# Performance work log

Hardware: AMD Instinct MI355X
Metric: run time of the kernel (lower is better)

Reference implementation:

```python
import jax, jax.numpy as jnp
import numpy as np

V, N, C, H, W = 4, 65536, 128, 512, 512
M_POOL, K, DH = 1024, 5, 128


def setup_inputs() -> dict:
    key = jax.random.key(0)
    ks = jax.random.split(key, 6)
    points = jax.random.normal(ks[0], (N, 3), dtype=jnp.float32) * 0.3  # human-scale pcd near origin
    zbuffer = 2.0 + jax.random.uniform(ks[1], (V, 1, H, W), dtype=jnp.float32)  # depth ~ camera distance
    feat_map = jax.random.normal(ks[2], (V, C, H, W), dtype=jnp.float32) * 0.1
    image = jax.random.uniform(ks[3], (V, 3, H, W), dtype=jnp.float32)
    # cameras: identity rotation, small x-baseline, looking at origin from z=2.5
    R = jnp.tile(jnp.eye(3, dtype=jnp.float32)[None], (V, 1, 1))
    t = jnp.stack([jnp.array([0.1 * v - 0.15, 0.0, 2.5], dtype=jnp.float32) for v in range(V)])
    extr = jnp.concatenate([R, t[:, :, None]], axis=-1)  # [V,3,4]
    intr = jnp.tile(jnp.array([[700.0, 0.0, W / 2], [0.0, 700.0, H / 2], [0.0, 0.0, 1.0]], dtype=jnp.float32)[None], (V, 1, 1))
    W1 = jax.random.normal(ks[4], (C + 1, DH), dtype=jnp.float32) * 0.05
    b1 = jnp.zeros((DH,), dtype=jnp.float32)
    w2 = jax.random.normal(ks[5], (DH, 1), dtype=jnp.float32) * 0.05
    return dict(points=points, extr=extr, intr=intr, zbuffer=zbuffer,
                feat_map=feat_map, image=image, W1=W1, b1=b1, w2=w2)


def _bilinear(img, u, v):
    """Zero-padded bilinear sample. img [C,H,W]; u,v [N] pixel coords -> [N,C]."""
    Cc, Hh, Ww = img.shape
    u0f = jnp.floor(u); v0f = jnp.floor(v)
    du = u - u0f; dv = v - v0f
    u0 = u0f.astype(jnp.int32); v0 = v0f.astype(jnp.int32)
    out = jnp.zeros((Cc, u.shape[0]), dtype=img.dtype)
    for vi, ui, w in ((v0, u0, (1 - du) * (1 - dv)), (v0, u0 + 1, du * (1 - dv)),
                      (v0 + 1, u0, (1 - du) * dv), (v0 + 1, u0 + 1, du * dv)):
        valid = ((vi >= 0) & (vi < Hh) & (ui >= 0) & (ui < Ww)).astype(img.dtype)
        vals = img[:, jnp.clip(vi, 0, Hh - 1), jnp.clip(ui, 0, Ww - 1)]  # [C,N]
        out = out + vals * (w * valid)[None]
    return out.T  # [N,C]


def _project(points, extr, intr):
    cam = jnp.einsum('vij,nj->vni', extr[:, :, :3], points) + extr[:, None, :, 3]  # [V,N,3]
    depth = cam[..., 2]  # [V,N]
    pix = jnp.einsum('vij,vnj->vni', intr, cam)
    u = pix[..., 0] / (pix[..., 2] + 1e-9)
    v = pix[..., 1] / (pix[..., 2] + 1e-9)
    return u, v, depth


def reference(points, extr, intr, zbuffer, feat_map, image, W1, b1, w2):
    u, v, depth = _project(points, extr, intr)
    sample = jax.vmap(_bilinear)  # over V views
    zbuf = sample(zbuffer, u, v)[..., 0]  # [V,N] sampled z-buffer (0 outside frame)
    out_mask = jnp.any(zbuf == 0.0, axis=0)  # [N] point missing in some view
    # --- KNN inverse-distance zbuf replacement (torch.no_grad block) ---
    pts_sg = jax.lax.stop_gradient(points)
    zbuf_sg = jax.lax.stop_gradient(zbuf)
    cand = pts_sg[:M_POOL]                       # candidate in-point pool
    cand_bad = out_mask[:M_POOL]
    d2 = jnp.sum((pts_sg[:, None, :] - cand[None, :, :]) ** 2, axis=-1)  # [N,M]
    d2 = jnp.where(cand_bad[None, :], jnp.inf, d2)
    negd, idx = jax.lax.top_k(-d2, K)            # K nearest candidates
    dists = jnp.sqrt(jnp.maximum(-negd, 0.0))
    disp = 1.0 / (dists + 1e-8)
    wknn = disp / (jnp.sum(disp, -1, keepdims=True) + 1e-12)  # [N,K]
    replace = jnp.sum(zbuf_sg[:, idx] * wknn[None], -1)       # [V,N]
    zbuf = jnp.where(out_mask[None], replace, zbuf)
    # --- visibility ---
    vis = 1.0 - jnp.abs(zbuf - depth) / (zbuf + 1e-9)  # [V,N]
    # --- multi-view projector sampling + attention fusion (MVF) ---
    feat_s = sample(feat_map, u, v)  # [V,N,C]
    rgb_s = sample(image, u, v)      # [V,N,3]
    x = jnp.concatenate([feat_s, vis[..., None]], -1)          # [V,N,C+1]
    h = jax.nn.relu(jnp.einsum('vnc,cd->vnd', x, W1) + b1)     # [V,N,DH]
    attn = jax.nn.softmax(jnp.einsum('vnd,do->vno', h, w2), axis=0)  # softmax over views
    feat = jnp.sum(attn * feat_s, axis=0)  # [N,C]
    rgb = jnp.sum(attn * rgb_s, axis=0)    # [N,3]
    return jnp.concatenate([feat, rgb], axis=-1)  # [N,C+3]
```

## Files before the change

### kernel.cpp

```cpp
#include <hip/hip_runtime.h>
#include <math.h>

#define NV 4
#define NPT 65536
#define NC 128
#define IMH 512
#define IMW 512
#define MPOOL 1024
#define NDH 128
#define KNN 5
#define NB 4
#define OUTC 131

typedef unsigned int uint32;
typedef unsigned short ushort16;
typedef __attribute__((ext_vector_type(8))) short short8v;
typedef __attribute__((ext_vector_type(4))) float float4v;

__device__ inline ushort16 f2bf(float f) {
    uint32 u = __float_as_uint(f);
    u += 0x7fffu + ((u >> 16) & 1u);
    return (ushort16)(u >> 16);
}
__device__ inline float bflo(uint32 a) { return __uint_as_float(a << 16); }
__device__ inline float bfhi(uint32 a) { return __uint_as_float(a & 0xffff0000u); }
__device__ inline float bf1(ushort16 a) { return __uint_as_float(((uint32)a) << 16); }

__global__ void k_wprep(const float* __restrict__ W1, uint4* __restrict__ Bf,
                        int* __restrict__ counter) {
    int idx = blockIdx.x * blockDim.x + threadIdx.x;
    if (idx == 0) *counter = 0;
    if (idx >= 5 * 8 * 64) return;
    int l = idx & 63, t = (idx >> 6) & 7, kb = idx >> 9;
    int d = t * 16 + (l & 15);
    uint32 w[4];
#pragma unroll
    for (int p = 0; p < 4; ++p) {
        uint32 lohi = 0;
#pragma unroll
        for (int h = 0; h < 2; ++h) {
            int j = p * 2 + h;
            int k = kb * 32 + (l >> 4) * 8 + j;
            float wv = (k < NC + 1) ? W1[k * NDH + d] : 0.f;
            lohi |= ((uint32)f2bf(wv)) << (16 * h);
        }
        w[p] = lohi;
    }
    Bf[idx] = make_uint4(w[0], w[1], w[2], w[3]);
}

__global__ __launch_bounds__(256)
void k_prep(const float* __restrict__ pts, const float* __restrict__ extr,
            const float* __restrict__ intr, const float* __restrict__ zbuffer,
            float* __restrict__ uarr, float* __restrict__ varr,
            float* __restrict__ darr, float* __restrict__ zarr,
            int* __restrict__ mask, int* __restrict__ list,
            int* __restrict__ counter) {
    int n = blockIdx.x * blockDim.x + threadIdx.x;
    if (n >= NPT) return;
    float p0 = pts[3 * n], p1 = pts[3 * n + 1], p2 = pts[3 * n + 2];
    int msk = 0;
#pragma unroll
    for (int v = 0; v < NV; ++v) {
        const float* e = extr + v * 12;
        float c0 = e[0] * p0 + e[1] * p1 + e[2] * p2 + e[3];
        float c1 = e[4] * p0 + e[5] * p1 + e[6] * p2 + e[7];
        float c2 = e[8] * p0 + e[9] * p1 + e[10] * p2 + e[11];
        const float* kk = intr + v * 9;
        float x0 = kk[0] * c0 + kk[1] * c1 + kk[2] * c2;
        float x1 = kk[3] * c0 + kk[4] * c1 + kk[5] * c2;
        float x2 = kk[6] * c0 + kk[7] * c1 + kk[8] * c2;
        float uu = x0 / (x2 + 1e-9f);
        float vv = x1 / (x2 + 1e-9f);
        int vn = v * NPT + n;
        uarr[vn] = uu; varr[vn] = vv; darr[vn] = c2;

        const float* img = zbuffer + (size_t)v * IMH * IMW;
        float u0f = floorf(uu), v0f = floorf(vv);
        float du = uu - u0f, dv = vv - v0f;
        int iu0 = (int)u0f, iv0 = (int)v0f;
        float w00 = (1.f - du) * (1.f - dv);
        float w01 = du * (1.f - dv);
        float w10 = (1.f - du) * dv;
        float w11 = du * dv;
        int iu0c = min(max(iu0, 0), IMW - 1), iu1c = min(max(iu0 + 1, 0), IMW - 1);
        int iv0c = min(max(iv0, 0), IMH - 1), iv1c = min(max(iv0 + 1, 0), IMH - 1);
        float m00 = (iu0 >= 0 && iu0 < IMW && iv0 >= 0 && iv0 < IMH) ? w00 : 0.f;
        float m01 = (iu0 + 1 >= 0 && iu0 + 1 < IMW && iv0 >= 0 && iv0 < IMH) ? w01 : 0.f;
        float m10 = (iu0 >= 0 && iu0 < IMW && iv0 + 1 >= 0 && iv0 + 1 < IMH) ? w10 : 0.f;
        float m11 = (iu0 + 1 >= 0 && iu0 + 1 < IMW && iv0 + 1 >= 0 && iv0 + 1 < IMH) ? w11 : 0.f;
        float z = img[iv0c * IMW + iu0c] * m00 + img[iv0c * IMW + iu1c] * m01 +
                  img[iv1c * IMW + iu0c] * m10 + img[iv1c * IMW + iu1c] * m11;
        zarr[vn] = z;
        msk |= (z == 0.f);
    }
    mask[n] = msk;
    if (msk) {
        int pos = atomicAdd(counter, 1);
        list[pos] = n;
    }
}

__global__ __launch_bounds__(256)
void k_knn_c(const float* __restrict__ pts, const int* __restrict__ mask,
             const int* __restrict__ list, const int* __restrict__ counter,
             float* __restrict__ zarr) {
    __shared__ float cx[MPOOL], cy[MPOOL], cz[MPOOL];
    int count = *counter;
    if ((int)blockIdx.x * 256 >= count) return;
    for (int m = threadIdx.x; m < MPOOL; m += 256) {
        int bad = mask[m];
        cx[m] = bad ? INFINITY : pts[3 * m];
        cy[m] = pts[3 * m + 1];
        cz[m] = pts[3 * m + 2];
    }
    __syncthreads();
    int i = blockIdx.x * 256 + threadIdx.x;
    if (i >= count) return;
    int n = list[i];
    float px = pts[3 * n], py = pts[3 * n + 1], pz = pts[3 * n + 2];
    float bd[KNN];
    int bi[KNN];
#pragma unroll
    for (int k = 0; k < KNN; ++k) { bd[k] = INFINITY; bi[k] = 0; }
    for (int m = 0; m < MPOOL; ++m) {
        float dx = px - cx[m];
        float dy = py - cy[m];
        float dz = pz - cz[m];
        float d = dx * dx + dy * dy + dz * dz;
        int id = m;
#pragma unroll
        for (int k = 0; k < KNN; ++k) {
            if (d < bd[k]) {
                float td = bd[k]; int ti = bi[k];
                bd[k] = d; bi[k] = id;
                d = td; id = ti;
            }
        }
    }
    float disp[KNN];
    float s = 0.f;
#pragma unroll
    for (int k = 0; k < KNN; ++k) {
        float dist = sqrtf(fmaxf(bd[k], 0.f));
        disp[k] = 1.f / (dist + 1e-8f);
        s += disp[k];
    }
    float inv = 1.f / (s + 1e-12f);
#pragma unroll
    for (int v = 0; v < NV; ++v) {
        float r = 0.f;
#pragma unroll
        for (int k = 0; k < KNN; ++k) r += zarr[v * NPT + bi[k]] * (disp[k] * inv);
        zarr[v * NPT + n] = r;
    }
}

__global__ __launch_bounds__(256)
void k_tfeat(const float* __restrict__ feat, ushort16* __restrict__ tfeat) {
    __shared__ ushort16 tile[128][130];
    int bid = blockIdx.x;
    int xt = bid & 3;
    int y = (bid >> 2) & 511;
    int v = bid >> 11;
    int x0 = xt * 128;
    int lane = threadIdx.x & 63, wave = threadIdx.x >> 6;
    const size_t HW = (size_t)IMH * IMW;
    const float* src = feat + (size_t)v * NC * HW + (size_t)y * IMW + x0;
#pragma unroll
    for (int i = 0; i < 32; ++i) {
        int c = i * 4 + wave;
        float2 val = *(const float2*)(src + (size_t)c * HW + lane * 2);
        tile[lane * 2][c] = f2bf(val.x);
        tile[lane * 2 + 1][c] = f2bf(val.y);
    }
    __syncthreads();
    uint32* dst = (uint32*)tfeat + ((size_t)v * HW + (size_t)y * IMW + x0) * 64;
#pragma unroll
    for (int i = 0; i < 32; ++i) {
        int pix = i * 4 + wave;
        uint32 val = *(const uint32*)&tile[pix][2 * lane];
        dst[(size_t)pix * 64 + lane] = val;
    }
}

__global__ __launch_bounds__(256)
void k_trgb(const float* __restrict__ image, ushort16* __restrict__ trgb) {
    int bid = blockIdx.x;
    int xt = bid & 1, y = (bid >> 1) & 511, v = bid >> 10;
    int x = xt * 256 + threadIdx.x;
    const size_t HW = (size_t)IMH * IMW;
    size_t p = (size_t)y * IMW + x;
    const float* src = image + (size_t)v * 3 * HW;
    ushort4 o;
    o.x = f2bf(src[p]);
    o.y = f2bf(src[HW + p]);
    o.z = f2bf(src[2 * HW + p]);
    o.w = 0;
    *(ushort4*)(trgb + ((size_t)v * HW + p) * 4) = o;
}

__global__ __launch_bounds__(128)
void k_fused_m(const float* __restrict__ uarr, const float* __restrict__ varr,
               const float* __restrict__ darr, const float* __restrict__ zarr,
               const ushort16* __restrict__ tfeat, const ushort16* __restrict__ trgb,
               const uint4* __restrict__ Bf, const float* __restrict__ b1,
               const float* __restrict__ w2, float* __restrict__ out) {
    const int tid = threadIdx.x;
    const int n0 = blockIdx.x * NB;
    const size_t HW = (size_t)IMH * IMW;
    __shared__ ushort16 fs[16][168];
    __shared__ float rgbs[16][3];
    __shared__ int po[16][4];
    __shared__ float pm[16][4];
    __shared__ float viss[16];
    __shared__ float sc[16];
    __shared__ float red[16][2];

    if (tid < 16) {
        int nb = tid >> 2, v = tid & 3;
        int vn = v * NPT + n0 + nb;
        float uu = uarr[vn], vv = varr[vn];
        float u0f = floorf(uu), v0f = floorf(vv);
        float du = uu - u0f, dv = vv - v0f;
        int iu0 = (int)u0f, iv0 = (int)v0f;
        float w00 = (1.f - du) * (1.f - dv);
        float w01 = du * (1.f - dv);
        float w10 = (1.f - du) * dv;
        float w11 = du * dv;
        int iu0c = min(max(iu0, 0), IMW - 1), iu1c = min(max(iu0 + 1, 0), IMW - 1);
        int iv0c = min(max(iv0, 0), IMH - 1), iv1c = min(max(iv0 + 1, 0), IMH - 1);
        float m00 = (iu0 >= 0 && iu0 < IMW && iv0 >= 0 && iv0 < IMH) ? w00 : 0.f;
        float m01 = (iu0 + 1 < IMW && iu0 + 1 >= 0 && iv0 >= 0 && iv0 < IMH) ? w01 : 0.f;
        float m10 = (iu0 >= 0 && iu0 < IMW && iv0 + 1 < IMH && iv0 + 1 >= 0) ? w10 : 0.f;
        float m11 = (iu0 + 1 < IMW && iu0 + 1 >= 0 && iv0 + 1 < IMH && iv0 + 1 >= 0) ? w11 : 0.f;
        int o00 = iv0c * IMW + iu0c, o01 = iv0c * IMW + iu1c;
        int o10 = iv1c * IMW + iu0c, o11 = iv1c * IMW + iu1c;
        po[tid][0] = o00; po[tid][1] = o01; po[tid][2] = o10; po[tid][3] = o11;
        pm[tid][0] = m00; pm[tid][1] = m01; pm[tid][2] = m10; pm[tid][3] = m11;
        float z = zarr[vn], dd = darr[vn];
        float vis = 1.f - fabsf(z - dd) / (z + 1e-9f);
        viss[tid] = vis;
        fs[tid][128] = f2bf(vis);
        for (int k = 129; k < 168; ++k) fs[tid][k] = 0;
        const ushort16* rb = trgb + (size_t)v * HW * 4;
        float ar = 0.f, ag = 0.f, ab = 0.f;
        int oo[4] = {o00, o01, o10, o11};
        float mm[4] = {m00, m01, m10, m11};
#pragma unroll
        for (int k = 0; k < 4; ++k) {
            const ushort16* c = rb + (size_t)oo[k] * 4;
            ar += bf1(c[0]) * mm[k];
            ag += bf1(c[1]) * mm[k];
            ab += bf1(c[2]) * mm[k];
        }
        rgbs[tid][0] = ar; rgbs[tid][1] = ag; rgbs[tid][2] = ab;
    }
    __syncthreads();

    const uint32* T = (const uint32*)tfeat;
    int sub = tid >> 6, c2 = tid & 63;
#pragma unroll
    for (int i = 0; i < 8; ++i) {
        int q = i * 2 + sub;
        int v = q & 3;
        const uint32* Bv = T + (size_t)v * HW * 64;
        int o0 = po[q][0], o1 = po[q][1], o2 = po[q][2], o3 = po[q][3];
        float m0 = pm[q][0], m1 = pm[q][1], m2 = pm[q][2], m3 = pm[q][3];
        uint32 a0 = Bv[(size_t)o0 * 64 + c2];
        uint32 a1 = Bv[(size_t)o1 * 64 + c2];
        uint32 a2 = Bv[(size_t)o2 * 64 + c2];
        uint32 a3 = Bv[(size_t)o3 * 64 + c2];
        float lo = bflo(a0) * m0 + bflo(a1) * m1 + bflo(a2) * m2 + bflo(a3) * m3;
        float hi = bfhi(a0) * m0 + bfhi(a1) * m1 + bfhi(a2) * m2 + bfhi(a3) * m3;
        uint32 packed = (uint32)f2bf(lo) | ((uint32)f2bf(hi) << 16);
        *(uint32*)&fs[q][2 * c2] = packed;
    }
    __syncthreads();

    const int l = tid & 63, w = tid >> 6;
    const int mrow = l & 15, kg = l >> 4;
    float4v acc[4];
#pragma unroll
    for (int t = 0; t < 4; ++t) acc[t] = (float4v){0.f, 0.f, 0.f, 0.f};
#pragma unroll
    for (int kb = 0; kb < 5; ++kb) {
        short8v av = *(const short8v*)&fs[mrow][kb * 32 + kg * 8];
#pragma unroll
        for (int tt = 0; tt < 4; ++tt) {
            int t = w * 4 + tt;
            short8v bv = *(const short8v*)&Bf[(kb * 8 + t) * 64 + l];
            acc[tt] = __builtin_amdgcn_mfma_f32_16x16x32_bf16(av, bv, acc[tt], 0, 0, 0);
        }
    }
    float bias[4], w2v[4];
#pragma unroll
    for (int tt = 0; tt < 4; ++tt) {
        int d = (w * 4 + tt) * 16 + mrow;
        bias[tt] = b1[d];
        w2v[tt] = w2[d];
    }
    float p[4] = {0.f, 0.f, 0.f, 0.f};
#pragma unroll
    for (int tt = 0; tt < 4; ++tt)
#pragma unroll
        for (int r = 0; r < 4; ++r)
            p[r] += fmaxf(acc[tt][r] + bias[tt], 0.f) * w2v[tt];
#pragma unroll
    for (int m = 1; m < 16; m <<= 1)
#pragma unroll
        for (int r = 0; r < 4; ++r) p[r] += __shfl_xor(p[r], m);
    if (mrow == 0) {
#pragma unroll
        for (int r = 0; r < 4; ++r) red[kg * 4 + r][w] = p[r];
    }
    __syncthreads();
    if (tid < 16) sc[tid] = red[tid][0] + red[tid][1];
    __syncthreads();
    if (tid < NB) {
        float s0 = sc[tid * 4 + 0], s1 = sc[tid * 4 + 1];
        float s2 = sc[tid * 4 + 2], s3 = sc[tid * 4 + 3];
        float mx = fmaxf(fmaxf(s0, s1), fmaxf(s2, s3));
        float e0 = expf(s0 - mx), e1 = expf(s1 - mx);
        float e2 = expf(s2 - mx), e3 = expf(s3 - mx);
        float inv = 1.f / (e0 + e1 + e2 + e3);
        sc[tid * 4 + 0] = e0 * inv; sc[tid * 4 + 1] = e1 * inv;
        sc[tid * 4 + 2] = e2 * inv; sc[tid * 4 + 3] = e3 * inv;
    }
    __syncthreads();

#pragma unroll
    for (int nb = 0; nb < NB; ++nb) {
        int n = n0 + nb;
        float f = 0.f;
#pragma unroll
        for (int v = 0; v < NV; ++v) f += sc[nb * 4 + v] * bf1(fs[nb * 4 + v][tid]);
        out[(size_t)n * OUTC + tid] = f;
        if (tid < 3) {
            float r = 0.f;
#pragma unroll
            for (int v = 0; v < NV; ++v) r += sc[nb * 4 + v] * rgbs[nb * 4 + v][tid];
            out[(size_t)n * OUTC + NC + tid] = r;
        }
    }
}

__global__ __launch_bounds__(128)
void k_fused_d(const float* __restrict__ uarr, const float* __restrict__ varr,
               const float* __restrict__ darr, const float* __restrict__ zarr,
               const float* __restrict__ feat, const float* __restrict__ image,
               const float* __restrict__ W1, const float* __restrict__ b1,
               const float* __restrict__ w2, float* __restrict__ out) {
    const int tid = threadIdx.x;
    const int n0 = blockIdx.x * NB;
    __shared__ float fs[NB][NV][NC];
    __shared__ float rgbs[NB][NV][3];
    __shared__ float sc[NB][NV];
    __shared__ float red[NB][NV][2];
    float vis[NB][NV];

#pragma unroll
    for (int nb = 0; nb < NB; ++nb) {
        int n = n0 + nb;
#pragma unroll
        for (int v = 0; v < NV; ++v) {
            int vn = v * NPT + n;
            float uu = uarr[vn], vv = varr[vn];
            float u0f = floorf(uu), v0f = floorf(vv);
            float du = uu - u0f, dv = vv - v0f;
            int iu0 = (int)u0f, iv0 = (int)v0f;
            float w00 = (1.f - du) * (1.f - dv);
            float w01 = du * (1.f - dv);
            float w10 = (1.f - du) * dv;
            float w11 = du * dv;
            int iu0c = min(max(iu0, 0), IMW - 1), iu1c = min(max(iu0 + 1, 0), IMW - 1);
            int iv0c = min(max(iv0, 0), IMH - 1), iv1c = min(max(iv0 + 1, 0), IMH - 1);
            float m00 = (iu0 >= 0 && iu0 < IMW && iv0 >= 0 && iv0 < IMH) ? w00 : 0.f;
            float m01 = (iu0 + 1 < IMW && iu0 + 1 >= 0 && iv0 >= 0 && iv0 < IMH) ? w01 : 0.f;
            float m10 = (iu0 >= 0 && iu0 < IMW && iv0 + 1 < IMH && iv0 + 1 >= 0) ? w10 : 0.f;
            float m11 = (iu0 + 1 < IMW && iu0 + 1 >= 0 && iv0 + 1 < IMH && iv0 + 1 >= 0) ? w11 : 0.f;
            int o00 = iv0c * IMW + iu0c, o01 = iv0c * IMW + iu1c;
            int o10 = iv1c * IMW + iu0c, o11 = iv1c * IMW + iu1c;
            const float* base = feat + ((size_t)(v * NC + tid)) * IMH * IMW;
            fs[nb][v][tid] = base[o00] * m00 + base[o01] * m01 +
                             base[o10] * m10 + base[o11] * m11;
            if (tid < 3) {
                const float* ib = image + ((size_t)(v * 3 + tid)) * IMH * IMW;
                rgbs[nb][v][tid] = ib[o00] * m00 + ib[o01] * m01 +
                                   ib[o10] * m10 + ib[o11] * m11;
            }
            float z = zarr[vn], dd = darr[vn];
            vis[nb][v] = 1.f - fabsf(z - dd) / (z + 1e-9f);
        }
    }
    __syncthreads();

    float h[NB][NV];
    float bv = b1[tid];
#pragma unroll
    for (int nb = 0; nb < NB; ++nb)
#pragma unroll
        for (int v = 0; v < NV; ++v) h[nb][v] = bv;
    for (int c = 0; c < NC; ++c) {
        float w = W1[c * NDH + tid];
#pragma unroll
        for (int nb = 0; nb < NB; ++nb)
#pragma unroll
            for (int v = 0; v < NV; ++v) h[nb][v] = fmaf(fs[nb][v][c], w, h[nb][v]);
    }
    {
        float w = W1[NC * NDH + tid];
#pragma unroll
        for (int nb = 0; nb < NB; ++nb)
#pragma unroll
            for (int v = 0; v < NV; ++v) h[nb][v] = fmaf(vis[nb][v], w, h[nb][v]);
    }
    float w2t = w2[tid];
    int lane = tid & 63, wave = tid >> 6;
#pragma unroll
    for (int nb = 0; nb < NB; ++nb) {
#pragma unroll
        for (int v = 0; v < NV; ++v) {
            float p = fmaxf(h[nb][v], 0.f) * w2t;
#pragma unroll
            for (int off = 32; off > 0; off >>= 1) p += __shfl_down(p, off);
            if (lane == 0) red[nb][v][wave] = p;
        }
    }
    __syncthreads();
    if (tid < NB * NV) {
        int nb = tid >> 2, v = tid & 3;
        sc[nb][v] = red[nb][v][0] + red[nb][v][1];
    }
    __syncthreads();
    if (tid < NB) {
        float s0 = sc[tid][0], s1 = sc[tid][1], s2 = sc[tid][2], s3 = sc[tid][3];
        float mx = fmaxf(fmaxf(s0, s1), fmaxf(s2, s3));
        float e0 = expf(s0 - mx), e1 = expf(s1 - mx);
        float e2 = expf(s2 - mx), e3 = expf(s3 - mx);
        float inv = 1.f / (e0 + e1 + e2 + e3);
        sc[tid][0] = e0 * inv; sc[tid][1] = e1 * inv;
        sc[tid][2] = e2 * inv; sc[tid][3] = e3 * inv;
    }
    __syncthreads();
#pragma unroll
    for (int nb = 0; nb < NB; ++nb) {
        int n = n0 + nb;
        float f = 0.f;
#pragma unroll
        for (int v = 0; v < NV; ++v) f += sc[nb][v] * fs[nb][v][tid];
        out[(size_t)n * OUTC + tid] = f;
        if (tid < 3) {
            float r = 0.f;
#pragma unroll
            for (int v = 0; v < NV; ++v) r += sc[nb][v] * rgbs[nb][v][tid];
            out[(size_t)n * OUTC + NC + tid] = r;
        }
    }
}

extern "C" void kernel_launch(void* const* d_in, const int* in_sizes, int n_in,
                              void* d_out, int out_size, void* d_ws, size_t ws_size,
                              hipStream_t stream) {
    const float* pts = (const float*)d_in[0];
    const float* extr = (const float*)d_in[1];
    const float* intr = (const float*)d_in[2];
    const float* zbuffer = (const float*)d_in[3];
    const float* feat = (const float*)d_in[4];
    const float* image = (const float*)d_in[5];
    const float* W1 = (const float*)d_in[6];
    const float* b1 = (const float*)d_in[7];
    const float* w2 = (const float*)d_in[8];
    float* out = (float*)d_out;

    const size_t VN = (size_t)NV * NPT;
    float* uarr = (float*)d_ws;
    float* varr = uarr + VN;
    float* darr = varr + VN;
    float* zarr = darr + VN;
    int* mask = (int*)(zarr + VN);
    int* list = mask + NPT;
    int* counter = list + NPT;
    uint4* Bf = (uint4*)(counter + 16);
    char* after = (char*)(Bf + 5 * 8 * 64);
    ushort16* trgb = (ushort16*)after;
    ushort16* tfeat = (ushort16*)(after + (size_t)NV * IMH * IMW * 4 * 2);
    size_t need = (size_t)((char*)tfeat - (char*)d_ws) + (size_t)NV * IMH * IMW * NC * 2;

    k_wprep<<<10, 256, 0, stream>>>(W1, Bf, counter);
    k_prep<<<NPT / 256, 256, 0, stream>>>(pts, extr, intr, zbuffer,
                                          uarr, varr, darr, zarr,
                                          mask, list, counter);
    k_knn_c<<<NPT / 256, 256, 0, stream>>>(pts, mask, list, counter, zarr);

    if (ws_size >= need) {
        k_tfeat<<<NV * 512 * 4, 256, 0, stream>>>(feat, tfeat);
        k_trgb<<<NV * 512 * 2, 256, 0, stream>>>(image, trgb);
        k_fused_m<<<NPT / NB, 128, 0, stream>>>(uarr, varr, darr, zarr, tfeat, trgb,
                                                Bf, b1, w2, out);
    } else {
        k_fused_d<<<NPT / NB, 128, 0, stream>>>(uarr, varr, darr, zarr, feat, image,
                                                W1, b1, w2, out);
    }
}
```

Measured before the change: 467.7 us.

## Skip transposing unreferenced feature tiles and double points per fused block

The prep kernel now marks which 128-pixel row segments of each view are touched by any bilinear corner. The feature transpose kernel then exits early for segments nobody samples, which avoids reading and converting most of the 512x512x128 feature map when points project into a small region. The fused MFMA kernel also handles 8 points per block instead of 4, using two 16-row MFMA groups, and spreads the per-sample corner setup across all threads with shuffle reductions. In exchange, the prep kernel gains scattered flag writes and the fused kernel needs more LDS and more registers.

```diff
diff --git a/kernel.cpp b/kernel.cpp
--- a/kernel.cpp
+++ b/kernel.cpp
@@ -9,8 +9,9 @@
 #define MPOOL 1024
 #define NDH 128
 #define KNN 5
-#define NB 4
+#define NB 8
 #define OUTC 131
+#define NFLAGS (4 * 512 * 4)
 
 typedef unsigned int uint32;
 typedef unsigned short ushort16;
@@ -27,9 +28,10 @@
 __device__ inline float bf1(ushort16 a) { return __uint_as_float(((uint32)a) << 16); }
 
 __global__ void k_wprep(const float* __restrict__ W1, uint4* __restrict__ Bf,
-                        int* __restrict__ counter) {
+                        int* __restrict__ counter, int* __restrict__ flags) {
     int idx = blockIdx.x * blockDim.x + threadIdx.x;
     if (idx == 0) *counter = 0;
+    if (idx < NFLAGS) flags[idx] = 0;
     if (idx >= 5 * 8 * 64) return;
     int l = idx & 63, t = (idx >> 6) & 7, kb = idx >> 9;
     int d = t * 16 + (l & 15);
@@ -55,7 +57,7 @@
             float* __restrict__ uarr, float* __restrict__ varr,
             float* __restrict__ darr, float* __restrict__ zarr,
             int* __restrict__ mask, int* __restrict__ list,
-            int* __restrict__ counter) {
+            int* __restrict__ counter, int* __restrict__ flags) {
     int n = blockIdx.x * blockDim.x + threadIdx.x;
     if (n >= NPT) return;
     float p0 = pts[3 * n], p1 = pts[3 * n + 1], p2 = pts[3 * n + 2];
@@ -93,6 +95,13 @@
                   img[iv1c * IMW + iu0c] * m10 + img[iv1c * IMW + iu1c] * m11;
         zarr[vn] = z;
         msk |= (z == 0.f);
+
+        int base = v * 2048;
+        int xt0 = iu0c >> 7, xt1 = iu1c >> 7;
+        flags[base + iv0c * 4 + xt0] = 1;
+        flags[base + iv0c * 4 + xt1] = 1;
+        flags[base + iv1c * 4 + xt0] = 1;
+        flags[base + iv1c * 4 + xt1] = 1;
     }
     mask[n] = msk;
     if (msk) {
@@ -157,12 +166,14 @@
 }
 
 __global__ __launch_bounds__(256)
-void k_tfeat(const float* __restrict__ feat, ushort16* __restrict__ tfeat) {
+void k_tfeat(const float* __restrict__ feat, ushort16* __restrict__ tfeat,
+             const int* __restrict__ flags) {
     __shared__ ushort16 tile[128][130];
     int bid = blockIdx.x;
     int xt = bid & 3;
     int y = (bid >> 2) & 511;
     int v = bid >> 11;
+    if (!flags[v * 2048 + y * 4 + xt]) return;
     int x0 = xt * 128;
     int lane = threadIdx.x & 63, wave = threadIdx.x >> 6;
     const size_t HW = (size_t)IMH * IMW;
@@ -209,16 +220,16 @@
     const int tid = threadIdx.x;
     const int n0 = blockIdx.x * NB;
     const size_t HW = (size_t)IMH * IMW;
-    __shared__ ushort16 fs[16][168];
-    __shared__ float rgbs[16][3];
-    __shared__ int po[16][4];
-    __shared__ float pm[16][4];
-    __shared__ float viss[16];
-    __shared__ float sc[16];
-    __shared__ float red[16][2];
-
-    if (tid < 16) {
-        int nb = tid >> 2, v = tid & 3;
+    __shared__ ushort16 fs[32][168];
+    __shared__ float rgbs[32][3];
+    __shared__ int po[32][4];
+    __shared__ float pm[32][4];
+    __shared__ float sc[32];
+    __shared__ float red[32][2];
+
+    {
+        int q = tid >> 2, corner = tid & 3;
+        int nb = q >> 2, v = q & 3;
         int vn = v * NPT + n0 + nb;
         float uu = uarr[vn], vv = varr[vn];
         float u0f = floorf(uu), v0f = floorf(vv);
@@ -234,34 +245,34 @@
         float m01 = (iu0 + 1 < IMW && iu0 + 1 >= 0 && iv0 >= 0 && iv0 < IMH) ? w01 : 0.f;
         float m10 = (iu0 >= 0 && iu0 < IMW && iv0 + 1 < IMH && iv0 + 1 >= 0) ? w10 : 0.f;
         float m11 = (iu0 + 1 < IMW && iu0 + 1 >= 0 && iv0 + 1 < IMH && iv0 + 1 >= 0) ? w11 : 0.f;
-        int o00 = iv0c * IMW + iu0c, o01 = iv0c * IMW + iu1c;
-        int o10 = iv1c * IMW + iu0c, o11 = iv1c * IMW + iu1c;
-        po[tid][0] = o00; po[tid][1] = o01; po[tid][2] = o10; po[tid][3] = o11;
-        pm[tid][0] = m00; pm[tid][1] = m01; pm[tid][2] = m10; pm[tid][3] = m11;
-        float z = zarr[vn], dd = darr[vn];
-        float vis = 1.f - fabsf(z - dd) / (z + 1e-9f);
-        viss[tid] = vis;
-        fs[tid][128] = f2bf(vis);
-        for (int k = 129; k < 168; ++k) fs[tid][k] = 0;
-        const ushort16* rb = trgb + (size_t)v * HW * 4;
-        float ar = 0.f, ag = 0.f, ab = 0.f;
-        int oo[4] = {o00, o01, o10, o11};
-        float mm[4] = {m00, m01, m10, m11};
-#pragma unroll
-        for (int k = 0; k < 4; ++k) {
-            const ushort16* c = rb + (size_t)oo[k] * 4;
-            ar += bf1(c[0]) * mm[k];
-            ag += bf1(c[1]) * mm[k];
-            ab += bf1(c[2]) * mm[k];
-        }
-        rgbs[tid][0] = ar; rgbs[tid][1] = ag; rgbs[tid][2] = ab;
+        int oo, iuc, ivc;
+        float mm;
+        if (corner == 0)      { ivc = iv0c; iuc = iu0c; mm = m00; }
+        else if (corner == 1) { ivc = iv0c; iuc = iu1c; mm = m01; }
+        else if (corner == 2) { ivc = iv1c; iuc = iu0c; mm = m10; }
+        else                  { ivc = iv1c; iuc = iu1c; mm = m11; }
+        oo = ivc * IMW + iuc;
+        po[q][corner] = oo;
+        pm[q][corner] = mm;
+        const ushort16* c = trgb + ((size_t)v * HW + oo) * 4;
+        float cr = bf1(c[0]) * mm, cg = bf1(c[1]) * mm, cb = bf1(c[2]) * mm;
+        cr += __shfl_xor(cr, 1); cr += __shfl_xor(cr, 2);
+        cg += __shfl_xor(cg, 1); cg += __shfl_xor(cg, 2);
+        cb += __shfl_xor(cb, 1); cb += __shfl_xor(cb, 2);
+        if (corner == 0) {
+            rgbs[q][0] = cr; rgbs[q][1] = cg; rgbs[q][2] = cb;
+            float z = zarr[vn], dd = darr[vn];
+            float vis = 1.f - fabsf(z - dd) / (z + 1e-9f);
+            fs[q][128] = f2bf(vis);
+        }
+        for (int k = 129 + corner; k < 168; k += 4) fs[q][k] = 0;
     }
     __syncthreads();
 
     const uint32* T = (const uint32*)tfeat;
     int sub = tid >> 6, c2 = tid & 63;
 #pragma unroll
-    for (int i = 0; i < 8; ++i) {
+    for (int i = 0; i < 16; ++i) {
         int q = i * 2 + sub;
         int v = q & 3;
         const uint32* Bv = T + (size_t)v * HW * 64;
@@ -279,43 +290,53 @@
     __syncthreads();
 
     const int l = tid & 63, w = tid >> 6;
-    const int mrow = l & 15, kg = l >> 4;
-    float4v acc[4];
-#pragma unroll
-    for (int t = 0; t < 4; ++t) acc[t] = (float4v){0.f, 0.f, 0.f, 0.f};
+    const int col = l & 15, kg = l >> 4;
+    float4v acc[2][4];
+#pragma unroll
+    for (int g = 0; g < 2; ++g)
+#pragma unroll
+        for (int t = 0; t < 4; ++t) acc[g][t] = (float4v){0.f, 0.f, 0.f, 0.f};
 #pragma unroll
     for (int kb = 0; kb < 5; ++kb) {
-        short8v av = *(const short8v*)&fs[mrow][kb * 32 + kg * 8];
+        short8v a0 = *(const short8v*)&fs[col][kb * 32 + kg * 8];
+        short8v a1 = *(const short8v*)&fs[16 + col][kb * 32 + kg * 8];
 #pragma unroll
         for (int tt = 0; tt < 4; ++tt) {
             int t = w * 4 + tt;
             short8v bv = *(const short8v*)&Bf[(kb * 8 + t) * 64 + l];
-            acc[tt] = __builtin_amdgcn_mfma_f32_16x16x32_bf16(av, bv, acc[tt], 0, 0, 0);
+            acc[0][tt] = __builtin_amdgcn_mfma_f32_16x16x32_bf16(a0, bv, acc[0][tt], 0, 0, 0);
+            acc[1][tt] = __builtin_amdgcn_mfma_f32_16x16x32_bf16(a1, bv, acc[1][tt], 0, 0, 0);
         }
     }
     float bias[4], w2v[4];
 #pragma unroll
     for (int tt = 0; tt < 4; ++tt) {
-        int d = (w * 4 + tt) * 16 + mrow;
+        int d = (w * 4 + tt) * 16 + col;
         bias[tt] = b1[d];
         w2v[tt] = w2[d];
     }
-    float p[4] = {0.f, 0.f, 0.f, 0.f};
-#pragma unroll
-    for (int tt = 0; tt < 4; ++tt)
-#pragma unroll
-        for (int r = 0; r < 4; ++r)
-            p[r] += fmaxf(acc[tt][r] + bias[tt], 0.f) * w2v[tt];
+    float p[2][4] = {{0.f, 0.f, 0.f, 0.f}, {0.f, 0.f, 0.f, 0.f}};
+#pragma unroll
+    for (int g = 0; g < 2; ++g)
+#pragma unroll
+        for (int tt = 0; tt < 4; ++tt)
+#pragma unroll
+            for (int r = 0; r < 4; ++r)
+                p[g][r] += fmaxf(acc[g][tt][r] + bias[tt], 0.f) * w2v[tt];
 #pragma unroll
     for (int m = 1; m < 16; m <<= 1)
 #pragma unroll
-        for (int r = 0; r < 4; ++r) p[r] += __shfl_xor(p[r], m);
-    if (mrow == 0) {
-#pragma unroll
-        for (int r = 0; r < 4; ++r) red[kg * 4 + r][w] = p[r];
-    }
-    __syncthreads();
-    if (tid < 16) sc[tid] = red[tid][0] + red[tid][1];
+        for (int g = 0; g < 2; ++g)
+#pragma unroll
+            for (int r = 0; r < 4; ++r) p[g][r] += __shfl_xor(p[g][r], m);
+    if (col == 0) {
+#pragma unroll
+        for (int g = 0; g < 2; ++g)
+#pragma unroll
+            for (int r = 0; r < 4; ++r) red[g * 16 + kg * 4 + r][w] = p[g][r];
+    }
+    __syncthreads();
+    if (tid < 32) sc[tid] = red[tid][0] + red[tid][1];
     __syncthreads();
     if (tid < NB) {
         float s0 = sc[tid * 4 + 0], s1 = sc[tid * 4 + 1];
@@ -352,15 +373,15 @@
                const float* __restrict__ W1, const float* __restrict__ b1,
                const float* __restrict__ w2, float* __restrict__ out) {
     const int tid = threadIdx.x;
-    const int n0 = blockIdx.x * NB;
-    __shared__ float fs[NB][NV][NC];
-    __shared__ float rgbs[NB][NV][3];
-    __shared__ float sc[NB][NV];
-    __shared__ float red[NB][NV][2];
-    float vis[NB][NV];
-
-#pragma unroll
-    for (int nb = 0; nb < NB; ++nb) {
+    const int n0 = blockIdx.x * 4;
+    __shared__ float fs[4][NV][NC];
+    __shared__ float rgbs[4][NV][3];
+    __shared__ float sc[4][NV];
+    __shared__ float red[4][NV][2];
+    float vis[4][NV];
+
+#pragma unroll
+    for (int nb = 0; nb < 4; ++nb) {
         int n = n0 + nb;
 #pragma unroll
         for (int v = 0; v < NV; ++v) {
@@ -395,30 +416,30 @@
     }
     __syncthreads();
 
-    float h[NB][NV];
+    float h[4][NV];
     float bv = b1[tid];
 #pragma unroll
-    for (int nb = 0; nb < NB; ++nb)
+    for (int nb = 0; nb < 4; ++nb)
 #pragma unroll
         for (int v = 0; v < NV; ++v) h[nb][v] = bv;
     for (int c = 0; c < NC; ++c) {
         float w = W1[c * NDH + tid];
 #pragma unroll
-        for (int nb = 0; nb < NB; ++nb)
+        for (int nb = 0; nb < 4; ++nb)
 #pragma unroll
             for (int v = 0; v < NV; ++v) h[nb][v] = fmaf(fs[nb][v][c], w, h[nb][v]);
     }
     {
         float w = W1[NC * NDH + tid];
 #pragma unroll
-        for (int nb = 0; nb < NB; ++nb)
+        for (int nb = 0; nb < 4; ++nb)
 #pragma unroll
             for (int v = 0; v < NV; ++v) h[nb][v] = fmaf(vis[nb][v], w, h[nb][v]);
     }
     float w2t = w2[tid];
     int lane = tid & 63, wave = tid >> 6;
 #pragma unroll
-    for (int nb = 0; nb < NB; ++nb) {
+    for (int nb = 0; nb < 4; ++nb) {
 #pragma unroll
         for (int v = 0; v < NV; ++v) {
             float p = fmaxf(h[nb][v], 0.f) * w2t;
@@ -428,12 +449,12 @@
         }
     }
     __syncthreads();
-    if (tid < NB * NV) {
+    if (tid < 16) {
         int nb = tid >> 2, v = tid & 3;
         sc[nb][v] = red[nb][v][0] + red[nb][v][1];
     }
     __syncthreads();
-    if (tid < NB) {
+    if (tid < 4) {
         float s0 = sc[tid][0], s1 = sc[tid][1], s2 = sc[tid][2], s3 = sc[tid][3];
         float mx = fmaxf(fmaxf(s0, s1), fmaxf(s2, s3));
         float e0 = expf(s0 - mx), e1 = expf(s1 - mx);
@@ -444,7 +465,7 @@
     }
     __syncthreads();
 #pragma unroll
-    for (int nb = 0; nb < NB; ++nb) {
+    for (int nb = 0; nb < 4; ++nb) {
         int n = n0 + nb;
         float f = 0.f;
 #pragma unroll
@@ -481,25 +502,26 @@
     int* mask = (int*)(zarr + VN);
     int* list = mask + NPT;
     int* counter = list + NPT;
-    uint4* Bf = (uint4*)(counter + 16);
+    int* flags = counter + 16;
+    uint4* Bf = (uint4*)(flags + NFLAGS);
     char* after = (char*)(Bf + 5 * 8 * 64);
     ushort16* trgb = (ushort16*)after;
     ushort16* tfeat = (ushort16*)(after + (size_t)NV * IMH * IMW * 4 * 2);
     size_t need = (size_t)((char*)tfeat - (char*)d_ws) + (size_t)NV * IMH * IMW * NC * 2;
 
-    k_wprep<<<10, 256, 0, stream>>>(W1, Bf, counter);
+    k_wprep<<<32, 256, 0, stream>>>(W1, Bf, counter, flags);
     k_prep<<<NPT / 256, 256, 0, stream>>>(pts, extr, intr, zbuffer,
                                           uarr, varr, darr, zarr,
-                                          mask, list, counter);
+                                          mask, list, counter, flags);
     k_knn_c<<<NPT / 256, 256, 0, stream>>>(pts, mask, list, counter, zarr);
 
     if (ws_size >= need) {
-        k_tfeat<<<NV * 512 * 4, 256, 0, stream>>>(feat, tfeat);
+        k_tfeat<<<NV * 512 * 4, 256, 0, stream>>>(feat, tfeat, flags);
         k_trgb<<<NV * 512 * 2, 256, 0, stream>>>(image, trgb);
         k_fused_m<<<NPT / NB, 128, 0, stream>>>(uarr, varr, darr, zarr, tfeat, trgb,
                                                 Bf, b1, w2, out);
     } else {
-        k_fused_d<<<NPT / NB, 128, 0, stream>>>(uarr, varr, darr, zarr, feat, image,
-                                                W1, b1, w2, out);
-    }
-}
+        k_fused_d<<<NPT / 4, 128, 0, stream>>>(uarr, varr, darr, zarr, feat, image,
+                                               W1, b1, w2, out);
+    }
+}
```

Result: no change. 468.9 us (+0.3%).
